# Performance work log

Measured on AMD Instinct MI355X. Metric: run time of the kernel, lower is better.

## Reference

```python
import jax, jax.numpy as jnp
import numpy as np

N_NODES = 100000
FIELD_DIM = 128
EMBED_DIM = 64
N_EDGES = 3200000
BATCH = 8192
NUM_FIELDS = 2


def setup_inputs() -> dict:
    key = jax.random.key(0)
    k1, k2, k3, k4 = jax.random.split(key, 4)
    features = jax.random.normal(k1, (N_NODES, FIELD_DIM), dtype=jnp.float32)
    edge_index = jax.random.randint(k2, (2, N_EDGES), 0, N_NODES, dtype=jnp.int32)
    # GCNConv linear weight (Glorot-ish scale) and bias
    W = jax.random.normal(k3, (FIELD_DIM, EMBED_DIM), dtype=jnp.float32) * (1.0 / np.sqrt(FIELD_DIM))
    bias = jnp.zeros((EMBED_DIM,), dtype=jnp.float32)
    x = jax.random.randint(k4, (BATCH, NUM_FIELDS), 0, N_NODES, dtype=jnp.int32)
    return {"features": features, "edge_index": edge_index, "W": W, "bias": bias, "x": x}


def reference(features, edge_index, W, bias, x):
    # GCNConv: out = D^{-1/2} (A + I) D^{-1/2} (X W) + b, then gather rows by x.
    n = features.shape[0]
    loop = jnp.arange(n, dtype=edge_index.dtype)
    src = jnp.concatenate([edge_index[0], loop])  # [E + N]
    dst = jnp.concatenate([edge_index[1], loop])  # [E + N]
    # degree (with self-loops) per destination node; >= 1 so rsqrt is safe
    deg = jax.ops.segment_sum(jnp.ones_like(dst, dtype=features.dtype), dst, num_segments=n)
    dinv = jax.lax.rsqrt(deg)
    norm = dinv[src] * dinv[dst]  # [E + N]
    h = features @ W  # [N, EMBED_DIM]
    msgs = h[src] * norm[:, None]  # gather + scale
    out = jax.ops.segment_sum(msgs, dst, num_segments=n) + bias  # [N, EMBED_DIM]
    return out[x]  # [BATCH, NUM_FIELDS, EMBED_DIM]
```

## Files before the change

### kernel.cpp

```cpp
#include <hip/hip_runtime.h>

#define N_NODES   100000
#define FIELD_DIM 128
#define EMBED_DIM 64
#define N_EDGES   3200000
#define NX        16384

#define NRANGE    4
#define RN        25000
#define RNH       12500
#define NSLICE    125
#define SLICE_E   (N_EDGES / NSLICE)
#define HISTB     (NRANGE * NSLICE)
#define GEMMB     ((N_NODES + 63) / 64)
#define FILLB     (N_EDGES / 4 / 256)

typedef short  bf16x8 __attribute__((ext_vector_type(8)));
typedef float  f32x4  __attribute__((ext_vector_type(4)));

__device__ __forceinline__ unsigned short f2bf(float x) {
    unsigned u = __float_as_uint(x);
    u += 0x7FFF + ((u >> 16) & 1);
    return (unsigned short)(u >> 16);
}
__device__ __forceinline__ float bf2f(unsigned short b) {
    return __uint_as_float(((unsigned)b) << 16);
}
__device__ __forceinline__ unsigned pk2(float lo, float hi) {
    return (unsigned)f2bf(lo) | ((unsigned)f2bf(hi) << 16);
}

__global__ void k_zero(float4* __restrict__ z4) {
    int i = blockIdx.x * blockDim.x + threadIdx.x;
    if (i < 784) z4[i] = make_float4(0.f, 0.f, 0.f, 0.f);
}

__global__ void k_init(const int* __restrict__ x, unsigned int* __restrict__ bits,
                       const float* __restrict__ W, unsigned short* __restrict__ Wt) {
    int b = blockIdx.x;
    if (b < 64) {
        int i = b * 256 + threadIdx.x;
        int v = x[i];
        atomicOr(&bits[v >> 5], 1u << (v & 31));
    } else {
        for (int i = threadIdx.x; i < FIELD_DIM * EMBED_DIM; i += 256) {
            int k = i >> 6, c = i & 63;
            Wt[c * FIELD_DIM + k] = f2bf(W[i]);
        }
    }
}

__global__ __launch_bounds__(256) void k_hist(const int* __restrict__ dst,
                                              unsigned int* __restrict__ partial32) {
    __shared__ unsigned int hist[RNH];
    int tid = threadIdx.x;
    int q = blockIdx.x & 3, s = blockIdx.x >> 2;
    for (int i = tid; i < RNH; i += 256) hist[i] = 0;
    __syncthreads();
    int lo = q * RN;
    const int4* dp = (const int4*)(dst + s * SLICE_E);
#pragma unroll
    for (int bt = 0; bt < 5; ++bt) {
        int4 d[5];
#pragma unroll
        for (int u = 0; u < 5; ++u) d[u] = dp[tid + 256 * (bt * 5 + u)];
#pragma unroll
        for (int u = 0; u < 5; ++u) {
            int a;
            a = d[u].x - lo; if ((unsigned)a < RN) atomicAdd(&hist[a >> 1], 1u << ((a & 1) << 4));
            a = d[u].y - lo; if ((unsigned)a < RN) atomicAdd(&hist[a >> 1], 1u << ((a & 1) << 4));
            a = d[u].z - lo; if ((unsigned)a < RN) atomicAdd(&hist[a >> 1], 1u << ((a & 1) << 4));
            a = d[u].w - lo; if ((unsigned)a < RN) atomicAdd(&hist[a >> 1], 1u << ((a & 1) << 4));
        }
    }
    __syncthreads();
    unsigned int* po = partial32 + (size_t)blockIdx.x * RNH;
    for (int i = tid; i < RNH; i += 256) po[i] = hist[i];
}

__global__ __launch_bounds__(256) void k_reduce(const unsigned int* __restrict__ partial32,
                                                const unsigned int* __restrict__ bits,
                                                int* __restrict__ cnt,
                                                float* __restrict__ dinv,
                                                int* __restrict__ nlist,
                                                int* __restrict__ inv,
                                                int* __restrict__ off,
                                                int* __restrict__ cur16,
                                                unsigned long long* __restrict__ counters) {
    __shared__ int wtot[4], wedge[4], ptot[4], pedge[4];
    __shared__ unsigned int baseN, baseE;
    int tid = threadIdx.x;
    int v = blockIdx.x * 256 + tid;
    bool inb = (v < N_NODES);
    int vc = inb ? v : (N_NODES - 1);
    int q = vc / RN, loc = vc - q * RN;
    int i2 = loc >> 1, sh = (loc & 1) << 4;
    const unsigned int* p = partial32 + (size_t)q * RNH + i2;
    int c = 0;
#pragma unroll
    for (int sb = 0; sb < 5; ++sb) {
        unsigned int vals[25];
#pragma unroll
        for (int s = 0; s < 25; ++s) vals[s] = p[(size_t)(sb * 25 + s) * (NRANGE * RNH)];
#pragma unroll
        for (int s = 0; s < 25; ++s) c += (int)((vals[s] >> sh) & 0xFFFFu);
    }
    if (inb) {
        cnt[v] = c;
        dinv[v] = rsqrtf((float)c + 1.0f);
    }
    bool fl = inb && ((bits[v >> 5] >> (v & 31)) & 1u);
    int lane = tid & 63;
    int w = tid >> 6;
    unsigned long long mask = __ballot(fl);
    int cc = fl ? c : 0;
    int incl = cc;
#pragma unroll
    for (int o = 1; o < 64; o <<= 1) {
        int t = __shfl_up(incl, o);
        if (lane >= o) incl += t;
    }
    if (lane == 63) { wtot[w] = __popcll(mask); wedge[w] = incl; }
    int myi = __popcll(mask & ((1ull << lane) - 1));
    int excl = incl - cc;
    __syncthreads();
    if (tid == 0) {
        int t0 = wtot[0], t1 = wtot[1], t2 = wtot[2], t3 = wtot[3];
        int e0 = wedge[0], e1 = wedge[1], e2 = wedge[2], e3 = wedge[3];
        ptot[0] = 0; ptot[1] = t0; ptot[2] = t0 + t1; ptot[3] = t0 + t1 + t2;
        pedge[0] = 0; pedge[1] = e0; pedge[2] = e0 + e1; pedge[3] = e0 + e1 + e2;
        int bt = t0 + t1 + t2 + t3;
        int be = e0 + e1 + e2 + e3;
        if (bt > 0) {
            unsigned long long add = ((unsigned long long)(unsigned)be << 32) |
                                     (unsigned long long)(unsigned)bt;
            unsigned long long old = atomicAdd(counters, add);
            baseN = (unsigned)(old & 0xFFFFFFFFull);
            baseE = (unsigned)(old >> 32);
        } else {
            baseN = 0; baseE = 0;
        }
    }
    __syncthreads();
    if (fl) {
        int i = (int)baseN + ptot[w] + myi;
        int o = (int)baseE + pedge[w] + excl;
        nlist[i] = v;
        inv[v] = i;
        off[v] = o;
        cur16[v << 4] = o;
    }
}

__global__ __launch_bounds__(256) void k_fillgemm(const int* __restrict__ src,
                                                  const int* __restrict__ dst,
                                                  const unsigned int* __restrict__ bits,
                                                  int* __restrict__ cur16,
                                                  int* __restrict__ elist,
                                                  const float* __restrict__ F,
                                                  const unsigned short* __restrict__ Wt,
                                                  unsigned short* __restrict__ h) {
    int b = blockIdx.x;
    int tid = threadIdx.x;
    bool isg = ((b % 3) == 0) && (b / 3 < GEMMB);
    if (!isg) {
        int fb = b - min(b / 3 + 1, GEMMB);
        int i = fb * 256 + tid;
        int4 d4 = ((const int4*)dst)[i];
        int4 s4 = ((const int4*)src)[i];
#define FILL1(dd, ss) if ((bits[(unsigned)(dd) >> 5] >> ((dd) & 31)) & 1u) \
        { int p = atomicAdd(&cur16[(dd) << 4], 1); elist[p] = ss; }
        FILL1(d4.x, s4.x)
        FILL1(d4.y, s4.y)
        FILL1(d4.z, s4.z)
        FILL1(d4.w, s4.w)
#undef FILL1
        return;
    }
    int gb = b / 3;
    int wave = tid >> 6, lane = tid & 63;
    int l15 = lane & 15, kg = lane >> 4;

    const char* wb = (const char*)Wt;
    bf16x8 bfrag[4][4];
#pragma unroll
    for (int cb = 0; cb < 4; ++cb)
#pragma unroll
        for (int ks = 0; ks < 4; ++ks)
            bfrag[cb][ks] = *(const bf16x8*)(wb + (cb * 16 + l15) * 256 + ks * 64 + kg * 16);

    int row = gb * 64 + wave * 16 + l15;
    int rowc = min(row, N_NODES - 1);
    const float4* F4 = (const float4*)(F + (size_t)rowc * FIELD_DIM + kg * 8);

    f32x4 acc[4];
#pragma unroll
    for (int cb = 0; cb < 4; ++cb) acc[cb] = (f32x4){0.f, 0.f, 0.f, 0.f};

#pragma unroll
    for (int ks = 0; ks < 4; ++ks) {
        float4 fa = F4[ks * 8];
        float4 fb = F4[ks * 8 + 1];
        union { bf16x8 v; unsigned u[4]; } af;
        af.u[0] = pk2(fa.x, fa.y);
        af.u[1] = pk2(fa.z, fa.w);
        af.u[2] = pk2(fb.x, fb.y);
        af.u[3] = pk2(fb.z, fb.w);
#pragma unroll
        for (int cb = 0; cb < 4; ++cb)
            acc[cb] = __builtin_amdgcn_mfma_f32_16x16x32_bf16(af.v, bfrag[cb][ks],
                                                              acc[cb], 0, 0, 0);
    }
    int rbase = gb * 64 + wave * 16 + kg * 4;
#pragma unroll
    for (int r = 0; r < 4; ++r) {
        int orow = rbase + r;
        if (orow < N_NODES) {
            unsigned short* hp = h + (size_t)orow * 64 + l15;
#pragma unroll
            for (int cb = 0; cb < 4; ++cb) hp[cb * 16] = f2bf(acc[cb][r]);
        }
    }
}

__global__ __launch_bounds__(256) void k_pull(const int* __restrict__ nlist,
                                              const int* __restrict__ counters,
                                              const int* __restrict__ cnt,
                                              const int* __restrict__ off,
                                              const int* __restrict__ elist,
                                              const unsigned short* __restrict__ h,
                                              const float* __restrict__ dinv,
                                              const float* __restrict__ bias,
                                              float* __restrict__ accc) {
    int t = blockIdx.x * blockDim.x + threadIdx.x;
    int wid = t >> 6;
    int lane = t & 63;
    if (wid >= counters[0]) return;
    int v = nlist[wid];
    float dvd = dinv[v];
    int deg = cnt[v];
    int base = off[v];
    float acc = bf2f(h[(size_t)v * 64 + lane]) * (dvd * dvd) + bias[lane];
    float acc2 = 0.f;
    int j = 0;
    for (; j + 7 < deg; j += 8) {
        int s0 = elist[base + j + 0];
        int s1 = elist[base + j + 1];
        int s2 = elist[base + j + 2];
        int s3 = elist[base + j + 3];
        int s4 = elist[base + j + 4];
        int s5 = elist[base + j + 5];
        int s6 = elist[base + j + 6];
        int s7 = elist[base + j + 7];
        float v0 = bf2f(h[(size_t)s0 * 64 + lane]);
        float v1 = bf2f(h[(size_t)s1 * 64 + lane]);
        float v2 = bf2f(h[(size_t)s2 * 64 + lane]);
        float v3 = bf2f(h[(size_t)s3 * 64 + lane]);
        float v4 = bf2f(h[(size_t)s4 * 64 + lane]);
        float v5 = bf2f(h[(size_t)s5 * 64 + lane]);
        float v6 = bf2f(h[(size_t)s6 * 64 + lane]);
        float v7 = bf2f(h[(size_t)s7 * 64 + lane]);
        float n0 = dinv[s0], n1 = dinv[s1], n2 = dinv[s2], n3 = dinv[s3];
        float n4 = dinv[s4], n5 = dinv[s5], n6 = dinv[s6], n7 = dinv[s7];
        acc  += v0 * (n0 * dvd);
        acc2 += v1 * (n1 * dvd);
        acc  += v2 * (n2 * dvd);
        acc2 += v3 * (n3 * dvd);
        acc  += v4 * (n4 * dvd);
        acc2 += v5 * (n5 * dvd);
        acc  += v6 * (n6 * dvd);
        acc2 += v7 * (n7 * dvd);
    }
    for (; j < deg; ++j) {
        int s0 = elist[base + j];
        acc += bf2f(h[(size_t)s0 * 64 + lane]) * (dinv[s0] * dvd);
    }
    accc[(size_t)wid * 64 + lane] = acc + acc2;
}

__global__ void k_gather(const int* __restrict__ x,
                         const int* __restrict__ inv,
                         const float* __restrict__ accc,
                         float* __restrict__ out) {
    int g = blockIdx.x * blockDim.x + threadIdx.x;
    if (g >= NX * 64) return;
    int v = x[g >> 6];
    out[g] = accc[(size_t)inv[v] * 64 + (g & 63)];
}

extern "C" void kernel_launch(void* const* d_in, const int* in_sizes, int n_in,
                              void* d_out, int out_size, void* d_ws, size_t ws_size,
                              hipStream_t stream) {
    const float* features = (const float*)d_in[0];
    const int*   edge     = (const int*)d_in[1];
    const float* W        = (const float*)d_in[2];
    const float* bias     = (const float*)d_in[3];
    const int*   x        = (const int*)d_in[4];
    float* out = (float*)d_out;

    char* ws = (char*)d_ws;
    unsigned short* h16      = (unsigned short*)(ws);
    unsigned int*   partial32= (unsigned int*)(ws + 12800000);
    int*            elist    = (int*)(ws + 12800000);
    float*          accc     = (float*)(ws + 37800000);
    int*            cnt      = (int*)  (ws + 41994304);
    float*          dinv     = (float*)(ws + 42394304);
    int*            off      = (int*)  (ws + 42794304);
    int*            inv      = (int*)  (ws + 43194304);
    int*            nlist    = (int*)  (ws + 43594304);
    unsigned long long* counters = (unsigned long long*)(ws + 43659840);
    unsigned int*   bits     = (unsigned int*) (ws + 43659872);
    unsigned short* Wt       = (unsigned short*)(ws + 43672384);
    int*            cur16    = (int*)  (ws + 43688768);

    const int* esrc = edge;
    const int* edst = edge + N_EDGES;

    k_zero    <<<4, 256, 0, stream>>>((float4*)(ws + 43659840));
    k_init    <<<65, 256, 0, stream>>>(x, bits, W, Wt);
    k_hist    <<<HISTB, 256, 0, stream>>>(edst, partial32);
    k_reduce  <<<(N_NODES + 255) / 256, 256, 0, stream>>>(partial32, bits, cnt, dinv,
                                                          nlist, inv, off, cur16, counters);
    k_fillgemm<<<FILLB + GEMMB, 256, 0, stream>>>(esrc, edst, bits, cur16, elist,
                                                  features, Wt, h16);
    k_pull    <<<(NX * 64 + 255) / 256, 256, 0, stream>>>(nlist, (const int*)counters,
                                                          cnt, off, elist, h16, dinv,
                                                          bias, accc);
    k_gather  <<<(NX * 64 + 255) / 256, 256, 0, stream>>>(x, inv, accc, out);
}
```

Baseline: 104.7 us.

## Replace global atomic edge fill with per-slice LDS cursors and precomputed slice bases

```diff
diff --git a/kernel.cpp b/kernel.cpp
--- a/kernel.cpp
+++ b/kernel.cpp
@@ -13,7 +13,7 @@
 #define SLICE_E   (N_EDGES / NSLICE)
 #define HISTB     (NRANGE * NSLICE)
 #define GEMMB     ((N_NODES + 63) / 64)
-#define FILLB     (N_EDGES / 4 / 256)
+#define SB_LD     16384
 
 typedef short  bf16x8 __attribute__((ext_vector_type(8)));
 typedef float  f32x4  __attribute__((ext_vector_type(4)));
@@ -85,7 +85,7 @@
                                                 int* __restrict__ nlist,
                                                 int* __restrict__ inv,
                                                 int* __restrict__ off,
-                                                int* __restrict__ cur16,
+                                                int* __restrict__ sbase,
                                                 unsigned long long* __restrict__ counters) {
     __shared__ int wtot[4], wedge[4], ptot[4], pedge[4];
     __shared__ unsigned int baseN, baseE;
@@ -142,42 +142,32 @@
         }
     }
     __syncthreads();
+    int ic = 0, oc = 0;
     if (fl) {
-        int i = (int)baseN + ptot[w] + myi;
-        int o = (int)baseE + pedge[w] + excl;
-        nlist[i] = v;
-        inv[v] = i;
-        off[v] = o;
-        cur16[v << 4] = o;
-    }
-}
-
-__global__ __launch_bounds__(256) void k_fillgemm(const int* __restrict__ src,
-                                                  const int* __restrict__ dst,
-                                                  const unsigned int* __restrict__ bits,
-                                                  int* __restrict__ cur16,
-                                                  int* __restrict__ elist,
-                                                  const float* __restrict__ F,
-                                                  const unsigned short* __restrict__ Wt,
-                                                  unsigned short* __restrict__ h) {
-    int b = blockIdx.x;
+        ic = (int)baseN + ptot[w] + myi;
+        oc = (int)baseE + pedge[w] + excl;
+        nlist[ic] = v;
+        inv[v] = ic;
+        off[v] = oc;
+    }
+    int cum = 0;
+#pragma unroll
+    for (int sb = 0; sb < 5; ++sb) {
+        unsigned int vals[25];
+#pragma unroll
+        for (int s = 0; s < 25; ++s) vals[s] = p[(size_t)(sb * 25 + s) * (NRANGE * RNH)];
+#pragma unroll
+        for (int s = 0; s < 25; ++s) {
+            if (fl) sbase[(size_t)(sb * 25 + s) * SB_LD + ic] = oc + cum;
+            cum += (int)((vals[s] >> sh) & 0xFFFFu);
+        }
+    }
+}
+
+__global__ __launch_bounds__(256) void k_gemm(const float* __restrict__ F,
+                                              const unsigned short* __restrict__ Wt,
+                                              unsigned short* __restrict__ h) {
     int tid = threadIdx.x;
-    bool isg = ((b % 3) == 0) && (b / 3 < GEMMB);
-    if (!isg) {
-        int fb = b - min(b / 3 + 1, GEMMB);
-        int i = fb * 256 + tid;
-        int4 d4 = ((const int4*)dst)[i];
-        int4 s4 = ((const int4*)src)[i];
-#define FILL1(dd, ss) if ((bits[(unsigned)(dd) >> 5] >> ((dd) & 31)) & 1u) \
-        { int p = atomicAdd(&cur16[(dd) << 4], 1); elist[p] = ss; }
-        FILL1(d4.x, s4.x)
-        FILL1(d4.y, s4.y)
-        FILL1(d4.z, s4.z)
-        FILL1(d4.w, s4.w)
-#undef FILL1
-        return;
-    }
-    int gb = b / 3;
     int wave = tid >> 6, lane = tid & 63;
     int l15 = lane & 15, kg = lane >> 4;
 
@@ -189,7 +179,7 @@
         for (int ks = 0; ks < 4; ++ks)
             bfrag[cb][ks] = *(const bf16x8*)(wb + (cb * 16 + l15) * 256 + ks * 64 + kg * 16);
 
-    int row = gb * 64 + wave * 16 + l15;
+    int row = blockIdx.x * 64 + wave * 16 + l15;
     int rowc = min(row, N_NODES - 1);
     const float4* F4 = (const float4*)(F + (size_t)rowc * FIELD_DIM + kg * 8);
 
@@ -211,7 +201,7 @@
             acc[cb] = __builtin_amdgcn_mfma_f32_16x16x32_bf16(af.v, bfrag[cb][ks],
                                                               acc[cb], 0, 0, 0);
     }
-    int rbase = gb * 64 + wave * 16 + kg * 4;
+    int rbase = blockIdx.x * 64 + wave * 16 + kg * 4;
 #pragma unroll
     for (int r = 0; r < 4; ++r) {
         int orow = rbase + r;
@@ -220,6 +210,36 @@
 #pragma unroll
             for (int cb = 0; cb < 4; ++cb) hp[cb * 16] = f2bf(acc[cb][r]);
         }
+    }
+}
+
+__global__ __launch_bounds__(1024) void k_fill(const int* __restrict__ src,
+                                               const int* __restrict__ dst,
+                                               const unsigned int* __restrict__ bits,
+                                               const int* __restrict__ inv,
+                                               const int* __restrict__ sbase,
+                                               int* __restrict__ elist) {
+    __shared__ unsigned int cur2[SB_LD / 2];
+    int s = blockIdx.x, tid = threadIdx.x;
+    for (int i = tid; i < SB_LD / 2; i += 1024) cur2[i] = 0;
+    __syncthreads();
+    const int4* dp = (const int4*)(dst + s * SLICE_E);
+    const int4* sp = (const int4*)(src + s * SLICE_E);
+    const int* sb = sbase + (size_t)s * SB_LD;
+    for (int it = tid; it < SLICE_E / 4; it += 1024) {
+        int4 d4 = dp[it];
+        int4 s4 = sp[it];
+#define FILL1(dd, ss) if ((bits[(unsigned)(dd) >> 5] >> ((dd) & 31)) & 1u) {      \
+        int ii = inv[dd];                                                          \
+        unsigned sh_ = (unsigned)((ii & 1) << 4);                                  \
+        unsigned old = atomicAdd(&cur2[ii >> 1], 1u << sh_);                       \
+        int idx = (int)((old >> sh_) & 0xFFFFu);                                   \
+        elist[sb[ii] + idx] = ss; }
+        FILL1(d4.x, s4.x)
+        FILL1(d4.y, s4.y)
+        FILL1(d4.z, s4.z)
+        FILL1(d4.w, s4.w)
+#undef FILL1
     }
 }
 
@@ -302,29 +322,29 @@
     unsigned short* h16      = (unsigned short*)(ws);
     unsigned int*   partial32= (unsigned int*)(ws + 12800000);
     int*            elist    = (int*)(ws + 12800000);
+    int*            sbase    = (int*)  (ws + 37800000);
     float*          accc     = (float*)(ws + 37800000);
-    int*            cnt      = (int*)  (ws + 41994304);
-    float*          dinv     = (float*)(ws + 42394304);
-    int*            off      = (int*)  (ws + 42794304);
-    int*            inv      = (int*)  (ws + 43194304);
-    int*            nlist    = (int*)  (ws + 43594304);
-    unsigned long long* counters = (unsigned long long*)(ws + 43659840);
-    unsigned int*   bits     = (unsigned int*) (ws + 43659872);
-    unsigned short* Wt       = (unsigned short*)(ws + 43672384);
-    int*            cur16    = (int*)  (ws + 43688768);
+    int*            cnt      = (int*)  (ws + 45992000);
+    float*          dinv     = (float*)(ws + 46392000);
+    int*            off      = (int*)  (ws + 46792000);
+    int*            inv      = (int*)  (ws + 47192000);
+    int*            nlist    = (int*)  (ws + 47592000);
+    unsigned long long* counters = (unsigned long long*)(ws + 47657536);
+    unsigned int*   bits     = (unsigned int*) (ws + 47657568);
+    unsigned short* Wt       = (unsigned short*)(ws + 47670080);
 
     const int* esrc = edge;
     const int* edst = edge + N_EDGES;
 
-    k_zero    <<<4, 256, 0, stream>>>((float4*)(ws + 43659840));
-    k_init    <<<65, 256, 0, stream>>>(x, bits, W, Wt);
-    k_hist    <<<HISTB, 256, 0, stream>>>(edst, partial32);
-    k_reduce  <<<(N_NODES + 255) / 256, 256, 0, stream>>>(partial32, bits, cnt, dinv,
-                                                          nlist, inv, off, cur16, counters);
-    k_fillgemm<<<FILLB + GEMMB, 256, 0, stream>>>(esrc, edst, bits, cur16, elist,
-                                                  features, Wt, h16);
-    k_pull    <<<(NX * 64 + 255) / 256, 256, 0, stream>>>(nlist, (const int*)counters,
-                                                          cnt, off, elist, h16, dinv,
-                                                          bias, accc);
-    k_gather  <<<(NX * 64 + 255) / 256, 256, 0, stream>>>(x, inv, accc, out);
-}
+    k_zero  <<<4, 256, 0, stream>>>((float4*)(ws + 47657536));
+    k_init  <<<65, 256, 0, stream>>>(x, bits, W, Wt);
+    k_hist  <<<HISTB, 256, 0, stream>>>(edst, partial32);
+    k_reduce<<<(N_NODES + 255) / 256, 256, 0, stream>>>(partial32, bits, cnt, dinv,
+                                                        nlist, inv, off, sbase, counters);
+    k_gemm  <<<GEMMB, 256, 0, stream>>>(features, Wt, h16);
+    k_fill  <<<NSLICE, 1024, 0, stream>>>(esrc, edst, bits, inv, sbase, elist);
+    k_pull  <<<(NX * 64 + 255) / 256, 256, 0, stream>>>(nlist, (const int*)counters,
+                                                        cnt, off, elist, h16, dinv,
+                                                        bias, accc);
+    k_gather<<<(NX * 64 + 255) / 256, 256, 0, stream>>>(x, inv, accc, out);
+}
```

Result: slower. 134.4 us (+28.4%).
